# Optimization experiments

Hardware: AMD Instinct MI355X
Metric: run time of the kernel (lower is better)

## Reference

```python
import jax, jax.numpy as jnp
import numpy as np

DIM = 2048
NUM_HEADS = 16
HEAD_DIM = DIM // NUM_HEADS  # 128
BATCH = 2
SEQ = 2048


def rope(x):
    # x: [B, S, H, Dh]; interleaved even/odd rotary embedding
    B, S, H, Dh = x.shape
    inv_freq = 1.0 / (10000.0 ** (jnp.arange(0, Dh, 2, dtype=jnp.float32) / Dh))  # [Dh/2]
    freqs = jnp.arange(S, dtype=jnp.float32)[:, None] * inv_freq[None, :]         # [S, Dh/2]
    cos = jnp.cos(freqs)[None, :, None, :]  # [1, S, 1, Dh/2]
    sin = jnp.sin(freqs)[None, :, None, :]
    x_even = x[..., 0::2]
    x_odd = x[..., 1::2]
    r_even = x_even * cos - x_odd * sin
    r_odd = x_even * sin + x_odd * cos
    # interleave back: [..., Dh/2, 2] -> [..., Dh]
    return jnp.stack([r_even, r_odd], axis=-1).reshape(x.shape)


def setup_inputs() -> dict:
    key = jax.random.key(0)
    ks = jax.random.split(key, 5)
    s = 1.0 / np.sqrt(DIM)
    return {
        "x": jax.random.normal(ks[0], (BATCH, SEQ, DIM), dtype=jnp.float32),
        "wq": jax.random.normal(ks[1], (DIM, DIM), dtype=jnp.float32) * s,
        "wk": jax.random.normal(ks[2], (DIM, DIM), dtype=jnp.float32) * s,
        "wv": jax.random.normal(ks[3], (DIM, DIM), dtype=jnp.float32) * s,
        "wo": jax.random.normal(ks[4], (DIM, DIM), dtype=jnp.float32) * s,
    }


def reference(x, wq, wk, wv, wo):
    B, S, D = x.shape
    H, Dh = NUM_HEADS, HEAD_DIM
    scale = Dh ** -0.5
    # nn.Linear(bias=False): y = x @ W.T
    q = (x @ wq.T).reshape(B, S, H, Dh)
    k = (x @ wk.T).reshape(B, S, H, Dh)
    v = (x @ wv.T).reshape(B, S, H, Dh)
    q = rope(q)
    k = rope(k)
    # no kv_cache -> new cache is (k, v) in [B, S, H, Dh] layout
    attn = jnp.einsum("bqhd,bkhd->bhqk", q, k) * scale  # [B, H, S, S]
    attn = jax.nn.softmax(attn, axis=-1)
    out = jnp.einsum("bhqk,bkhd->bqhd", attn, v).reshape(B, S, D)
    out = out @ wo.T
    return (out, k, v)
```

## Files before the change

kernel.cpp:

```cpp
#include <hip/hip_runtime.h>
#include <hip/hip_bf16.h>

#define DIM 2048
#define SEQLEN 2048
#define NHEADS 16
#define HDIM 128
#define NBATCH 2

using short8 = __attribute__((ext_vector_type(8))) short;
using f32x4 = __attribute__((ext_vector_type(4))) float;
using ushort4v = __attribute__((ext_vector_type(4))) unsigned short;

typedef __attribute__((address_space(1))) const void gvoid_t;
typedef __attribute__((address_space(3))) void lvoid_t;

__device__ __forceinline__ void gl_lds16(const void* g, void* l) {
  __builtin_amdgcn_global_load_lds((gvoid_t*)g, (lvoid_t*)l, 16, 0, 0);
}

__device__ __forceinline__ unsigned short f2bf(float f) {
  union { float f; unsigned int u; } v;
  v.f = f;
  unsigned int u = v.u;
  return (unsigned short)((u + 0x7FFFu + ((u >> 16) & 1u)) >> 16);
}

__device__ __forceinline__ f32x4 mfma16(short8 a, short8 b, f32x4 c) {
  return __builtin_amdgcn_mfma_f32_16x16x32_bf16(a, b, c, 0, 0, 0);
}

__global__ __launch_bounds__(256) void cast_all(
    const float4* __restrict__ x,
    const float4* __restrict__ wq, const float4* __restrict__ wk,
    const float4* __restrict__ wv, const float4* __restrict__ wo,
    ushort4v* __restrict__ xb,
    ushort4v* __restrict__ wqb, ushort4v* __restrict__ wkb,
    ushort4v* __restrict__ wvb, ushort4v* __restrict__ wob)
{
  const long NXV = 2097152;
  const long NWV = 1048576;
  long tid = (long)blockIdx.x * blockDim.x + threadIdx.x;
  long nth = (long)gridDim.x * blockDim.x;
  for (long i = tid; i < NXV + 4 * NWV; i += nth) {
    const float4* s; ushort4v* dst; long off;
    if (i < NXV) { s = x; dst = xb; off = i; }
    else {
      long j = i - NXV;
      int w = (int)(j >> 20);
      off = j & (NWV - 1);
      switch (w) {
        case 0:  s = wq; dst = wqb; break;
        case 1:  s = wk; dst = wkb; break;
        case 2:  s = wv; dst = wvb; break;
        default: s = wo; dst = wob; break;
      }
    }
    float4 f = s[off];
    ushort4v u;
    u.x = f2bf(f.x); u.y = f2bf(f.y); u.z = f2bf(f.z); u.w = f2bf(f.w);
    dst[off] = u;
  }
}

__global__ __launch_bounds__(256) void rope_tables(float* __restrict__ ctab,
                                                   float* __restrict__ stab)
{
  int idx = blockIdx.x * 256 + threadIdx.x;
  if (idx >= SEQLEN * 64) return;
  int s = idx >> 6, i = idx & 63;
  float inv = powf(10000.0f, -(float)(2 * i) * (1.0f / 128.0f));
  float a = (float)s * inv;
  ctab[idx] = cosf(a);
  stab[idx] = sinf(a);
}

template<bool ROPE, bool WF32, bool WBF16>
__global__ __launch_bounds__(256) void gemm_bt(
    const unsigned short* __restrict__ A,
    const unsigned short* __restrict__ B,
    float* __restrict__ Cf,
    unsigned short* __restrict__ Cb,
    int M, int N, int K,
    const float* __restrict__ ctab,
    const float* __restrict__ stab,
    float premul)
{
  __shared__ unsigned short As[128 * 32];
  __shared__ unsigned short Bs[128 * 32];
  const int tid = threadIdx.x;
  const int wv = tid >> 6;
  const int lane = tid & 63;
  const int q4 = lane >> 4;
  const int l15 = lane & 15;
  const int m0 = blockIdx.y * 128;
  const int n0 = blockIdx.x * 128;
  const int wy = wv >> 1, wx = wv & 1;

  f32x4 acc[4][4];
  for (int i = 0; i < 4; ++i)
    for (int j = 0; j < 4; ++j)
      acc[i][j] = f32x4{0.f, 0.f, 0.f, 0.f};

  for (int k0 = 0; k0 < K; k0 += 32) {
    for (int j = 0; j < 2; ++j) {
      int sb = wv * 128 + j * 64;
      int slot = sb + lane;
      int r = slot >> 2, c = slot & 3;
      gl_lds16(A + (size_t)(m0 + r) * K + k0 + c * 8, &As[sb * 8]);
      gl_lds16(B + (size_t)(n0 + r) * K + k0 + c * 8, &Bs[sb * 8]);
    }
    __syncthreads();
    short8 af[4], bf[4];
    for (int i = 0; i < 4; ++i)
      af[i] = *reinterpret_cast<const short8*>(&As[(wy * 64 + i * 16 + l15) * 32 + q4 * 8]);
    for (int j = 0; j < 4; ++j)
      bf[j] = *reinterpret_cast<const short8*>(&Bs[(wx * 64 + j * 16 + l15) * 32 + q4 * 8]);
    for (int i = 0; i < 4; ++i)
      for (int j = 0; j < 4; ++j)
        acc[i][j] = mfma16(af[i], bf[j], acc[i][j]);
    __syncthreads();
  }

  for (int i = 0; i < 4; ++i) {
    for (int j = 0; j < 4; ++j) {
      int colb = n0 + wx * 64 + j * 16 + l15;
      for (int r = 0; r < 4; ++r) {
        int row = m0 + wy * 64 + i * 16 + q4 * 4 + r;
        float val = acc[i][j][r];
        if (ROPE) {
          int s = row & (SEQLEN - 1);
          int pi = (colb & (HDIM - 1)) >> 1;
          float cs = ctab[(s << 6) + pi];
          float sn = stab[(s << 6) + pi];
          float partner = __shfl_xor(val, 1);
          val = (colb & 1) ? fmaf(partner, sn, val * cs)
                           : fmaf(val, cs, -partner * sn);
        }
        if (WF32) Cf[(size_t)row * N + colb] = val;
        if (WBF16) Cb[(size_t)row * N + colb] = f2bf(val * premul);
      }
    }
  }
}

__global__ __launch_bounds__(256) void transpose_v(const float* __restrict__ v,
                                                   unsigned short* __restrict__ vt)
{
  __shared__ float tile[64][65];
  const int b = blockIdx.z;
  const int s0 = blockIdx.y * 64;
  const int d0 = blockIdx.x * 64;
  const int tx = threadIdx.x & 63;
  const int ty = threadIdx.x >> 6;
  for (int r = 0; r < 16; ++r) {
    int srow = r * 4 + ty;
    tile[srow][tx] = v[((size_t)(b * SEQLEN + s0 + srow)) * DIM + d0 + tx];
  }
  __syncthreads();
  for (int r = 0; r < 16; ++r) {
    int drow = r * 4 + ty;
    int d = d0 + drow;
    int bh = b * NHEADS + (d >> 7);
    int dh = d & 127;
    vt[((size_t)(bh * HDIM + dh)) * SEQLEN + s0 + tx] = f2bf(tile[tx][drow]);
  }
}

__global__ __launch_bounds__(256, 4) void flash_attn(
    const unsigned short* __restrict__ qb,
    const unsigned short* __restrict__ kb,
    const unsigned short* __restrict__ vt,
    unsigned short* __restrict__ ab)
{
  __shared__ unsigned short KP[64 * 128];
  __shared__ unsigned short VTs[128 * 64];
  __shared__ unsigned short Ps[64 * 64];
  const int tid = threadIdx.x;
  const int wvi = tid >> 6;
  const int lane = tid & 63;
  const int q4 = lane >> 4;
  const int l15 = lane & 15;
  const int bh = blockIdx.x;
  const int q0 = blockIdx.y * 64;
  const int b = bh >> 4, h = bh & 15;

  const unsigned short* qbase = qb + (size_t)b * SEQLEN * DIM + h * HDIM;
  const unsigned short* kbase = kb + (size_t)b * SEQLEN * DIM + h * HDIM;
  const unsigned short* vbase = vt + (size_t)bh * HDIM * SEQLEN;

  short8 qf[4];
  {
    const unsigned short* qrow = qbase + (size_t)(q0 + wvi * 16 + l15) * DIM;
    for (int ks = 0; ks < 4; ++ks)
      qf[ks] = *reinterpret_cast<const short8*>(qrow + (ks * 4 + q4) * 8);
  }

  float m_run[4], l_run[4];
  f32x4 o[8];
  for (int r = 0; r < 4; ++r) { m_run[r] = -3.0e38f; l_run[r] = 0.f; }
  for (int ct = 0; ct < 8; ++ct) o[ct] = f32x4{0.f, 0.f, 0.f, 0.f};

  const int par = lane & 1;

  for (int kv = 0; kv < SEQLEN / 64; ++kv) {
    const int kv0 = kv * 64;
    for (int j = 0; j < 4; ++j) {
      int sb = wvi * 256 + j * 64;
      int slot = sb + lane;
      {
        int row = slot >> 4, cp = slot & 15;
        int c = cp ^ (row & 7);
        gl_lds16(kbase + (size_t)(kv0 + row) * DIM + c * 8, &KP[sb * 8]);
      }
      {
        int row = slot >> 3, cp = slot & 7;
        int c = cp ^ (row & 7);
        gl_lds16(vbase + (size_t)row * SEQLEN + kv0 + c * 8, &VTs[sb * 8]);
      }
    }
    __syncthreads();

    f32x4 sc[4];
    for (int ct = 0; ct < 4; ++ct) sc[ct] = f32x4{0.f, 0.f, 0.f, 0.f};
    for (int ct = 0; ct < 4; ++ct) {
      int kr = ct * 16 + l15;
      for (int ks = 0; ks < 4; ++ks) {
        int c = (ks * 4 + q4) ^ (kr & 7);
        short8 kf = *reinterpret_cast<const short8*>(&KP[kr * 128 + c * 8]);
        sc[ct] = mfma16(qf[ks], kf, sc[ct]);
      }
    }

    float lm[4];
    for (int r = 0; r < 4; ++r)
      lm[r] = fmaxf(fmaxf(sc[0][r], sc[1][r]), fmaxf(sc[2][r], sc[3][r]));
    bool grow = false;
    for (int r = 0; r < 4; ++r) grow |= (lm[r] > m_run[r] + 8.0f);
    if (__any(grow)) {
      for (int r = 0; r < 4; ++r) {
        float mx = lm[r];
        for (int d = 1; d < 16; d <<= 1) mx = fmaxf(mx, __shfl_xor(mx, d));
        float mnew = fmaxf(m_run[r], mx);
        float al = __builtin_amdgcn_exp2f(m_run[r] - mnew);
        m_run[r] = mnew;
        l_run[r] *= al;
        for (int ct = 0; ct < 8; ++ct) o[ct][r] *= al;
      }
    }

    for (int ct = 0; ct < 4; ++ct)
      for (int r = 0; r < 4; ++r) {
        float e = __builtin_amdgcn_exp2f(sc[ct][r] - m_run[r]);
        sc[ct][r] = e;
        l_run[r] += e;
      }

    for (int ct = 0; ct < 4; ++ct) {
      float t0 = __shfl_xor(sc[ct][0], 1);
      float t1 = __shfl_xor(sc[ct][1], 1);
      float t2 = __shfl_xor(sc[ct][2], 1);
      float t3 = __shfl_xor(sc[ct][3], 1);
      float a0 = par ? t2 : sc[ct][0];
      float b0 = par ? sc[ct][2] : t0;
      float a1 = par ? t3 : sc[ct][1];
      float b1 = par ? sc[ct][3] : t1;
      unsigned int pk0, pk1;
      asm("v_cvt_pk_bf16_f32 %0, %1, %2" : "=v"(pk0) : "v"(a0), "v"(b0));
      asm("v_cvt_pk_bf16_f32 %0, %1, %2" : "=v"(pk1) : "v"(a1), "v"(b1));
      int col0 = ct * 16 + (l15 & ~1);
      int prow0 = wvi * 16 + q4 * 4 + par * 2;
      int c0 = (col0 >> 3) ^ (prow0 & 7);
      *reinterpret_cast<unsigned int*>(&Ps[prow0 * 64 + c0 * 8 + (col0 & 7)]) = pk0;
      int prow1 = prow0 + 1;
      int c1 = (col0 >> 3) ^ (prow1 & 7);
      *reinterpret_cast<unsigned int*>(&Ps[prow1 * 64 + c1 * 8 + (col0 & 7)]) = pk1;
    }
    __asm__ volatile("s_waitcnt lgkmcnt(0)" ::: "memory");

    short8 pf[2];
    {
      int prow = wvi * 16 + l15;
      for (int ks = 0; ks < 2; ++ks) {
        int c = (ks * 4 + q4) ^ (prow & 7);
        pf[ks] = *reinterpret_cast<const short8*>(&Ps[prow * 64 + c * 8]);
      }
    }
    for (int ct = 0; ct < 8; ++ct) {
      int vr = ct * 16 + l15;
      for (int ks = 0; ks < 2; ++ks) {
        int c = (ks * 4 + q4) ^ (vr & 7);
        short8 vf = *reinterpret_cast<const short8*>(&VTs[vr * 64 + c * 8]);
        o[ct] = mfma16(pf[ks], vf, o[ct]);
      }
    }
    __syncthreads();
  }

  for (int r = 0; r < 4; ++r) {
    float t = l_run[r];
    for (int d = 1; d < 16; d <<= 1) t += __shfl_xor(t, d);
    float invl = 1.0f / t;
    int qrow = q0 + wvi * 16 + q4 * 4 + r;
    size_t base = ((size_t)(b * SEQLEN) + qrow) * DIM + h * HDIM;
    for (int ct = 0; ct < 8; ++ct)
      ab[base + ct * 16 + l15] = f2bf(o[ct][r] * invl);
  }
}

extern "C" void kernel_launch(void* const* d_in, const int* in_sizes, int n_in,
                              void* d_out, int out_size, void* d_ws, size_t ws_size,
                              hipStream_t stream) {
  const float* x  = (const float*)d_in[0];
  const float* wq = (const float*)d_in[1];
  const float* wk = (const float*)d_in[2];
  const float* wv = (const float*)d_in[3];
  const float* wo = (const float*)d_in[4];

  float* outp = (float*)d_out;
  float* kout = outp + 8388608;
  float* vout = outp + 16777216;

  unsigned short* ws  = (unsigned short*)d_ws;
  unsigned short* xb  = ws;
  unsigned short* wqb = xb + 8388608;
  unsigned short* wkb = wqb + 4194304;
  unsigned short* wvb = wkb + 4194304;
  unsigned short* wob = wvb + 4194304;
  unsigned short* qb  = wob + 4194304;
  unsigned short* kb  = qb + 8388608;
  unsigned short* vtb = kb + 8388608;
  unsigned short* abuf = vtb + 8388608;
  float* ctab = (float*)(abuf + 8388608);
  float* stab = ctab + 131072;

  cast_all<<<2048, 256, 0, stream>>>(
      (const float4*)x, (const float4*)wq, (const float4*)wk,
      (const float4*)wv, (const float4*)wo,
      (ushort4v*)xb, (ushort4v*)wqb, (ushort4v*)wkb,
      (ushort4v*)wvb, (ushort4v*)wob);
  rope_tables<<<512, 256, 0, stream>>>(ctab, stab);

  dim3 gg(16, 32);
  const float qscale = 0.08838834764831845f * 1.4426950408889634f;
  gemm_bt<true,  false, true ><<<gg, 256, 0, stream>>>(xb, wqb, nullptr, qb, 4096, 2048, 2048, ctab, stab, qscale);
  gemm_bt<true,  true,  true ><<<gg, 256, 0, stream>>>(xb, wkb, kout,    kb, 4096, 2048, 2048, ctab, stab, 1.0f);
  gemm_bt<false, true,  false><<<gg, 256, 0, stream>>>(xb, wvb, vout, nullptr, 4096, 2048, 2048, ctab, stab, 1.0f);

  transpose_v<<<dim3(32, 32, 2), 256, 0, stream>>>(vout, vtb);
  flash_attn<<<dim3(32, 32), 256, 0, stream>>>(qb, kb, vtb, abuf);

  gemm_bt<false, true,  false><<<gg, 256, 0, stream>>>(abuf, wob, outp, nullptr, 4096, 2048, 2048, ctab, stab, 1.0f);
}
```

Measured before the change: 523.5 us.

## Double-buffer GEMM LDS tiles with K=64 steps and XOR swizzle

The bf16 GEMM main loop now uses two LDS buffers so the global-to-LDS load of the next K tile is issued before computing on the current one, removing one barrier per step. The K tile grows from 32 to 64, halving loop iterations, and an XOR swizzle on the 16-byte chunk index spreads LDS reads across banks. This quadruples LDS use per block (64 KB), which may lower occupancy, and it relies on the single barrier being enough to order the async LDS writes against the reads.

```diff
diff --git a/kernel.cpp b/kernel.cpp
--- a/kernel.cpp
+++ b/kernel.cpp
@@ -85,8 +85,8 @@
     const float* __restrict__ stab,
     float premul)
 {
-  __shared__ unsigned short As[128 * 32];
-  __shared__ unsigned short Bs[128 * 32];
+  __shared__ unsigned short As[2][128 * 64];
+  __shared__ unsigned short Bs[2][128 * 64];
   const int tid = threadIdx.x;
   const int wv = tid >> 6;
   const int lane = tid & 63;
@@ -101,24 +101,44 @@
     for (int j = 0; j < 4; ++j)
       acc[i][j] = f32x4{0.f, 0.f, 0.f, 0.f};
 
-  for (int k0 = 0; k0 < K; k0 += 32) {
-    for (int j = 0; j < 2; ++j) {
-      int sb = wv * 128 + j * 64;
+  auto stage = [&](int buf, int k0) {
+    for (int j = 0; j < 4; ++j) {
+      int sb = j * 256 + wv * 64;
       int slot = sb + lane;
-      int r = slot >> 2, c = slot & 3;
-      gl_lds16(A + (size_t)(m0 + r) * K + k0 + c * 8, &As[sb * 8]);
-      gl_lds16(B + (size_t)(n0 + r) * K + k0 + c * 8, &Bs[sb * 8]);
-    }
+      int row = slot >> 3, cp = slot & 7;
+      int c = cp ^ (row & 7);
+      gl_lds16(A + (size_t)(m0 + row) * K + k0 + c * 8, &As[buf][sb * 8]);
+      gl_lds16(B + (size_t)(n0 + row) * K + k0 + c * 8, &Bs[buf][sb * 8]);
+    }
+  };
+
+  stage(0, 0);
+  __syncthreads();
+
+  int cur = 0;
+  for (int k0 = 0; k0 < K; k0 += 64) {
+    if (k0 + 64 < K) stage(cur ^ 1, k0 + 64);
+
+    short8 af[2][4], bf[2][4];
+    for (int s = 0; s < 2; ++s)
+      for (int i = 0; i < 4; ++i) {
+        int row = wy * 64 + i * 16 + l15;
+        int c = (s * 4 + q4) ^ (row & 7);
+        af[s][i] = *reinterpret_cast<const short8*>(&As[cur][row * 64 + c * 8]);
+      }
+    for (int s = 0; s < 2; ++s)
+      for (int j = 0; j < 4; ++j) {
+        int row = wx * 64 + j * 16 + l15;
+        int c = (s * 4 + q4) ^ (row & 7);
+        bf[s][j] = *reinterpret_cast<const short8*>(&Bs[cur][row * 64 + c * 8]);
+      }
+    for (int s = 0; s < 2; ++s)
+      for (int i = 0; i < 4; ++i)
+        for (int j = 0; j < 4; ++j)
+          acc[i][j] = mfma16(af[s][i], bf[s][j], acc[i][j]);
+
     __syncthreads();
-    short8 af[4], bf[4];
-    for (int i = 0; i < 4; ++i)
-      af[i] = *reinterpret_cast<const short8*>(&As[(wy * 64 + i * 16 + l15) * 32 + q4 * 8]);
-    for (int j = 0; j < 4; ++j)
-      bf[j] = *reinterpret_cast<const short8*>(&Bs[(wx * 64 + j * 16 + l15) * 32 + q4 * 8]);
-    for (int i = 0; i < 4; ++i)
-      for (int j = 0; j < 4; ++j)
-        acc[i][j] = mfma16(af[i], bf[j], acc[i][j]);
-    __syncthreads();
+    cur ^= 1;
   }
 
   for (int i = 0; i < 4; ++i) {
```

Measured after the change: 462.7 us. 1.13x faster.

## Triple-buffer GEMM K-loop with async LDS loads and enlarge flash-attn query tile

Applied to the files above, without the earlier changes.

The GEMM main loop now keeps three LDS buffers, prefetching two K-slices ahead with global_load_lds. Each iteration needs only one barrier, with a partial vmcnt wait, so global loads overlap the MFMA work. Flash attention moves to 512-thread blocks covering 128 query rows, so each K/V tile loaded into LDS is shared by twice as many waves, halving K/V reload traffic. The trade-offs are more LDS per block, possibly lower occupancy, and reliance on the hand-written waitcnt counts matching the two loads issued per stage.

```diff
diff --git a/kernel.cpp b/kernel.cpp
--- a/kernel.cpp
+++ b/kernel.cpp
@@ -85,8 +85,8 @@
     const float* __restrict__ stab,
     float premul)
 {
-  __shared__ unsigned short As[128 * 32];
-  __shared__ unsigned short Bs[128 * 32];
+  __shared__ unsigned short As[3][128 * 32];
+  __shared__ unsigned short Bs[3][128 * 32];
   const int tid = threadIdx.x;
   const int wv = tid >> 6;
   const int lane = tid & 63;
@@ -101,24 +101,45 @@
     for (int j = 0; j < 4; ++j)
       acc[i][j] = f32x4{0.f, 0.f, 0.f, 0.f};
 
-  for (int k0 = 0; k0 < K; k0 += 32) {
+  auto stage = [&](int buf, int k0) {
     for (int j = 0; j < 2; ++j) {
       int sb = wv * 128 + j * 64;
       int slot = sb + lane;
       int r = slot >> 2, c = slot & 3;
-      gl_lds16(A + (size_t)(m0 + r) * K + k0 + c * 8, &As[sb * 8]);
-      gl_lds16(B + (size_t)(n0 + r) * K + k0 + c * 8, &Bs[sb * 8]);
-    }
-    __syncthreads();
+      gl_lds16(A + (size_t)(m0 + r) * K + k0 + c * 8, &As[buf][sb * 8]);
+      gl_lds16(B + (size_t)(n0 + r) * K + k0 + c * 8, &Bs[buf][sb * 8]);
+    }
+  };
+
+  const int NT = K / 32;
+  stage(0, 0);
+  stage(1, 32);
+  asm volatile("s_waitcnt vmcnt(4)" ::: "memory");
+  __builtin_amdgcn_s_barrier();
+  __builtin_amdgcn_sched_barrier(0);
+
+  int cur = 0;
+  for (int t = 0; t < NT; ++t) {
+    if (t + 2 < NT) stage((t + 2) % 3, (t + 2) * 32);
+
     short8 af[4], bf[4];
     for (int i = 0; i < 4; ++i)
-      af[i] = *reinterpret_cast<const short8*>(&As[(wy * 64 + i * 16 + l15) * 32 + q4 * 8]);
+      af[i] = *reinterpret_cast<const short8*>(
+          &As[cur][(wy * 64 + i * 16 + l15) * 32 + q4 * 8]);
     for (int j = 0; j < 4; ++j)
-      bf[j] = *reinterpret_cast<const short8*>(&Bs[(wx * 64 + j * 16 + l15) * 32 + q4 * 8]);
+      bf[j] = *reinterpret_cast<const short8*>(
+          &Bs[cur][(wx * 64 + j * 16 + l15) * 32 + q4 * 8]);
     for (int i = 0; i < 4; ++i)
       for (int j = 0; j < 4; ++j)
         acc[i][j] = mfma16(af[i], bf[j], acc[i][j]);
-    __syncthreads();
+
+    if (t + 1 < NT) {
+      if (t + 2 < NT) asm volatile("s_waitcnt vmcnt(4)" ::: "memory");
+      else            asm volatile("s_waitcnt vmcnt(0)" ::: "memory");
+      __builtin_amdgcn_s_barrier();
+      __builtin_amdgcn_sched_barrier(0);
+    }
+    cur = (cur == 2) ? 0 : cur + 1;
   }
 
   for (int i = 0; i < 4; ++i) {
@@ -166,7 +187,7 @@
   }
 }
 
-__global__ __launch_bounds__(256, 4) void flash_attn(
+__global__ __launch_bounds__(512, 4) void flash_attn(
     const unsigned short* __restrict__ qb,
     const unsigned short* __restrict__ kb,
     const unsigned short* __restrict__ vt,
@@ -174,14 +195,14 @@
 {
   __shared__ unsigned short KP[64 * 128];
   __shared__ unsigned short VTs[128 * 64];
-  __shared__ unsigned short Ps[64 * 64];
+  __shared__ unsigned short Ps[128 * 64];
   const int tid = threadIdx.x;
   const int wvi = tid >> 6;
   const int lane = tid & 63;
   const int q4 = lane >> 4;
   const int l15 = lane & 15;
   const int bh = blockIdx.x;
-  const int q0 = blockIdx.y * 64;
+  const int q0 = blockIdx.y * 128;
   const int b = bh >> 4, h = bh & 15;
 
   const unsigned short* qbase = qb + (size_t)b * SEQLEN * DIM + h * HDIM;
@@ -204,8 +225,8 @@
 
   for (int kv = 0; kv < SEQLEN / 64; ++kv) {
     const int kv0 = kv * 64;
-    for (int j = 0; j < 4; ++j) {
-      int sb = wvi * 256 + j * 64;
+    for (int j = 0; j < 2; ++j) {
+      int sb = wvi * 128 + j * 64;
       int slot = sb + lane;
       {
         int row = slot >> 4, cp = slot & 15;
@@ -347,7 +368,7 @@
   gemm_bt<false, true,  false><<<gg, 256, 0, stream>>>(xb, wvb, vout, nullptr, 4096, 2048, 2048, ctab, stab, 1.0f);
 
   transpose_v<<<dim3(32, 32, 2), 256, 0, stream>>>(vout, vtb);
-  flash_attn<<<dim3(32, 32), 256, 0, stream>>>(qb, kb, vtb, abuf);
+  flash_attn<<<dim3(32, 16), 512, 0, stream>>>(qb, kb, vtb, abuf);
 
   gemm_bt<false, true,  false><<<gg, 256, 0, stream>>>(abuf, wob, outp, nullptr, 4096, 2048, 2048, ctab, stab, 1.0f);
 }
```

After: 504.6 us. -3.6%, faster.
